# Performance work log

Hardware: AMD Instinct MI355X
Metric: run time of the kernel (lower is better)

Reference implementation:

```python
import jax, jax.numpy as jnp
import numpy as np

H = 1024
F = 132

def _lstm_cell(x, h, c, Wih, Whh, bih, bhh):
    # PyTorch LSTMCell: gates ordered i, f, g, o
    gates = x @ Wih.T + bih + h @ Whh.T + bhh  # [B, 4H]
    i, f, g, o = jnp.split(gates, 4, axis=-1)
    i = jax.nn.sigmoid(i)
    f = jax.nn.sigmoid(f)
    g = jnp.tanh(g)
    o = jax.nn.sigmoid(o)
    c_new = f * c + i * g
    h_new = o * jnp.tanh(c_new)
    return h_new, c_new


def setup_inputs() -> dict:
    key = jax.random.key(0)
    ks = jax.random.split(key, 16)
    s = 0.02
    return {
        "initial_seq": jax.random.normal(ks[0], (32, 64, F), dtype=jnp.float32),
        "generate_frames_number": 128,
        "W_ih1": jax.random.normal(ks[1], (4 * H, F), dtype=jnp.float32) * s,
        "W_hh1": jax.random.normal(ks[2], (4 * H, H), dtype=jnp.float32) * s,
        "b_ih1": jax.random.normal(ks[3], (4 * H,), dtype=jnp.float32) * s,
        "b_hh1": jax.random.normal(ks[4], (4 * H,), dtype=jnp.float32) * s,
        "W_ih2": jax.random.normal(ks[5], (4 * H, H), dtype=jnp.float32) * s,
        "W_hh2": jax.random.normal(ks[6], (4 * H, H), dtype=jnp.float32) * s,
        "b_ih2": jax.random.normal(ks[7], (4 * H,), dtype=jnp.float32) * s,
        "b_hh2": jax.random.normal(ks[8], (4 * H,), dtype=jnp.float32) * s,
        "W_ih3": jax.random.normal(ks[9], (4 * H, H), dtype=jnp.float32) * s,
        "W_hh3": jax.random.normal(ks[10], (4 * H, H), dtype=jnp.float32) * s,
        "b_ih3": jax.random.normal(ks[11], (4 * H,), dtype=jnp.float32) * s,
        "b_hh3": jax.random.normal(ks[12], (4 * H,), dtype=jnp.float32) * s,
        "W_dec": jax.random.normal(ks[13], (F, H), dtype=jnp.float32) * s,
        "b_dec": jax.random.normal(ks[14], (F,), dtype=jnp.float32) * s,
    }


def reference(initial_seq, generate_frames_number,
              W_ih1, W_hh1, b_ih1, b_hh1,
              W_ih2, W_hh2, b_ih2, b_hh2,
              W_ih3, W_hh3, b_ih3, b_hh3,
              W_dec, b_dec):
    B = initial_seq.shape[0]
    dt = initial_seq.dtype
    zeros = jnp.zeros((B, H), dtype=dt)
    state0 = (zeros, zeros, zeros, zeros, zeros, zeros)  # h0,h1,h2,c0,c1,c2

    def step(state, in_frame):
        h0, h1, h2, c0, c1, c2 = state
        h0, c0 = _lstm_cell(in_frame, h0, c0, W_ih1, W_hh1, b_ih1, b_hh1)
        h1, c1 = _lstm_cell(h0, h1, c1, W_ih2, W_hh2, b_ih2, b_hh2)
        h2, c2 = _lstm_cell(h1, h2, c2, W_ih3, W_hh3, b_ih3, b_hh3)
        out_frame = h2 @ W_dec.T + b_dec  # [B, F]
        return (h0, h1, h2, c0, c1, c2), out_frame

    # Priming pass over the conditioning sequence (outputs discarded except last)
    def prime_step(carry, in_frame):
        state, _ = carry
        state, out = step(state, in_frame)
        return (state, out), None

    init_frame = jnp.zeros((B, F), dtype=dt)
    xs = jnp.swapaxes(initial_seq, 0, 1)  # [T, B, F]
    (state, cur_frame), _ = jax.lax.scan(prime_step, (state0, init_frame), xs)

    def gen_step(carry, _):
        state, frame = carry
        state, out = step(state, frame)
        return (state, out), out

    _, outs = jax.lax.scan(gen_step, (state, cur_frame), None,
                           length=generate_frames_number)  # [N, B, F]
    return jnp.swapaxes(outs, 0, 1)  # [B, N, F]
```

## Files before the change

kernel.cpp:

```cpp
#include <hip/hip_runtime.h>
#include <stdint.h>

typedef unsigned short u16;
typedef unsigned long long u64;
typedef __attribute__((ext_vector_type(8))) short short8;
typedef __attribute__((ext_vector_type(4))) float f32x4;

#define SZ_BIGW    (4096ull*1024ull*2ull)
#define OFF_WHH1   (0ull)
#define OFF_WIH2   (OFF_WHH1 + SZ_BIGW)
#define OFF_WHH2   (OFF_WIH2 + SZ_BIGW)
#define OFF_WIH3   (OFF_WHH2 + SZ_BIGW)
#define OFF_WHH3   (OFF_WIH3 + SZ_BIGW)
#define OFF_MCOMB  (OFF_WHH3 + SZ_BIGW)
#define OFF_WIH1   (OFF_MCOMB + SZ_BIGW)
#define SZ_WIH1    (4096ull*160ull*2ull)
#define OFF_WDECF  (OFF_WIH1 + SZ_WIH1)
#define SZ_WDECF   (160ull*1024ull*2ull)
#define OFF_WDECB  (OFF_WDECF + SZ_WDECF)
#define SZ_WDECB   (1024ull*160ull*2ull)
#define OFF_XPRIM  (OFF_WDECB + SZ_WDECB)
#define SZ_XPRIM   (64ull*5120ull*2ull)
#define OFF_H2HIST (OFF_XPRIM + SZ_XPRIM)
#define SZ_HSLOT   (32768ull*2ull)
#define SZ_H2HIST  (129ull*SZ_HSLOT)
#define OFF_H0R    (OFF_H2HIST + SZ_H2HIST)
#define SZ_HR      (192ull*SZ_HSLOT)
#define OFF_H1R    (OFF_H0R + SZ_HR)
#define OFF_H2R    (OFF_H1R + SZ_HR)
#define SZ_H2R     (64ull*SZ_HSLOT)
#define OFF_ZEROH  (OFF_H2R + SZ_H2R)
#define OFF_FLAGS  (OFF_ZEROH + SZ_HSLOT)
#define SZ_FLAGS   (4096ull)
#define OFF_BS1    (OFF_FLAGS + SZ_FLAGS)
#define OFF_BS1G   (OFF_BS1 + 16384ull)
#define OFF_BS2    (OFF_BS1G + 16384ull)
#define OFF_BS3    (OFF_BS2 + 16384ull)
#define BLOB_SIZE  (OFF_BS3 + 16384ull)

__device__ unsigned char g_blob[BLOB_SIZE];

#define ZERO_BYTES (SZ_HSLOT + SZ_FLAGS)

__device__ __forceinline__ u16 f2bf(float f) {
  unsigned u = __float_as_uint(f);
  u += 0x7fffu + ((u >> 16) & 1u);
  return (u16)(u >> 16);
}
__device__ __forceinline__ float sigm(float x) { return 1.f / (1.f + __expf(-x)); }
__device__ __forceinline__ float tanh_(float x) {
  x = fminf(fmaxf(x, -40.f), 40.f);
  float e = __expf(2.f * x);
  return (e - 1.f) / (e + 1.f);
}

__global__ __launch_bounds__(256) void k_zero(uint4* p, int n) {
  int i = blockIdx.x * 256 + threadIdx.x;
  for (; i < n; i += gridDim.x * 256) p[i] = make_uint4(0u, 0u, 0u, 0u);
}

__global__ __launch_bounds__(256) void k_swizzle(const float* __restrict__ src, u16* __restrict__ dst,
                                                 int J, int Jsrc, int Kpad, int Ksrc, int srcld,
                                                 int transposed, int perm) {
  int total = J * Kpad;
  int nkc = Kpad >> 3;
  for (int o = blockIdx.x * 256 + threadIdx.x; o < total; o += gridDim.x * 256) {
    int chunk = o >> 7, within = o & 127;
    int nt = chunk / nkc, kc = chunk - nt * nkc;
    int jr = within >> 3, ke = within & 7;
    int j = perm ? ((jr >> 2) * 1024 + nt * 4 + (jr & 3)) : (nt * 16 + jr);
    int k = kc * 8 + ke;
    float v = 0.f;
    if (j < Jsrc && k < Ksrc)
      v = transposed ? src[(size_t)k * srcld + j] : src[(size_t)j * srcld + k];
    dst[o] = f2bf(v);
  }
}

__global__ __launch_bounds__(256) void k_xprim(const float* __restrict__ iseq, u16* __restrict__ dst) {
  int o = blockIdx.x * 256 + threadIdx.x;
  if (o >= 64 * 5120) return;
  int t = o / 5120, rem = o - t * 5120;
  int kc = rem >> 8, b = (rem >> 3) & 31, ke = rem & 7;
  int k = kc * 8 + ke;
  float v = (k < 132) ? iseq[(size_t)b * (64 * 132) + t * 132 + k] : 0.f;
  dst[o] = f2bf(v);
}

__global__ __launch_bounds__(256) void k_bias(const float* bih1, const float* bhh1,
                                              const float* bih2, const float* bhh2,
                                              const float* bih3, const float* bhh3,
                                              const float* __restrict__ Wih1, const float* __restrict__ bdec,
                                              float* bs1, float* bs1g, float* bs2, float* bs3) {
  int j = blockIdx.x * 256 + threadIdx.x;
  if (j >= 4096) return;
  float s1 = bih1[j] + bhh1[j];
  float bc = 0.f;
  const float* wr = Wih1 + (size_t)j * 132;
  for (int f = 0; f < 132; ++f) bc += wr[f] * bdec[f];
  bs1[j] = s1;
  bs1g[j] = s1 + bc;
  bs2[j] = bih2[j] + bhh2[j];
  bs3[j] = bih3[j] + bhh3[j];
}

__global__ __launch_bounds__(256) void k_mcomb(const u16* __restrict__ A, const u16* __restrict__ Bm,
                                               u16* __restrict__ dst) {
  int blk = blockIdx.x;
  int mt = blk & 255, jg = blk >> 8;
  int w = threadIdx.x >> 6, l = threadIdx.x & 63, q = l >> 4, r = l & 15;
  int nt = jg * 4 + w;
  f32x4 acc = {};
  for (int ks = 0; ks < 5; ++ks) {
    short8 a = *(const short8*)(A + ((size_t)mt * 20 + ks * 4 + q) * 128 + r * 8);
    short8 b = *(const short8*)(Bm + ((size_t)nt * 20 + ks * 4 + q) * 128 + r * 8);
    acc = __builtin_amdgcn_mfma_f32_16x16x32_bf16(a, b, acc, 0, 0, 0);
  }
  int kout = nt * 16 + r;
#pragma unroll
  for (int i = 0; i < 4; ++i) {
    int jrow = q * 4 + i;
    dst[(((size_t)mt * 128 + (kout >> 3)) << 7) + jrow * 8 + (kout & 7)] = f2bf(acc[i]);
  }
}


__device__ __forceinline__ void wait_all(unsigned* F, unsigned tgt) {
  if (threadIdx.x < 256) {
    while (__hip_atomic_load(F + threadIdx.x, __ATOMIC_RELAXED, __HIP_MEMORY_SCOPE_AGENT) < tgt)
      __builtin_amdgcn_s_sleep(1);
  }
  __syncthreads();
}

#define MFMA(a, b, c) __builtin_amdgcn_mfma_f32_16x16x32_bf16((a), (b), (c), 0, 0, 0)

template<int LBASE>
__device__ __forceinline__ void gen_layer(
    const u16* __restrict__ xa, const short8 (&wA)[4],
    const u16* __restrict__ xb, const short8 (&wB)[4],
    unsigned* waitF, unsigned wtgt,
    const float* __restrict__ bsum, float& creg, u16* __restrict__ hout,
    unsigned* arrF, unsigned aval,
    float (*red)[2][256], u64* hstage, int nt)
{
  int tid = threadIdx.x;
  int w = tid >> 6, l = tid & 63, q = l >> 4, r = l & 15;
  f32x4 acc0 = {}, acc1 = {};

#pragma unroll
  for (int i = 0; i < 4; ++i) {
    const u16* xp = xb + (w + 8 * i) * 1024 + q * 256 + r * 8;
    short8 a0 = *(const short8*)(xp);
    short8 a1 = *(const short8*)(xp + 128);
    acc0 = MFMA(a0, wB[i], acc0);
    acc1 = MFMA(a1, wB[i], acc1);
  }

  wait_all(waitF, wtgt);

#pragma unroll
  for (int i = 0; i < 4; ++i) {
    const u16* xp = xa + (w + 8 * i) * 1024 + q * 256 + r * 8;
    short8 a0 = *(const short8*)(xp);
    short8 a1 = *(const short8*)(xp + 128);
    acc0 = MFMA(a0, wA[i], acc0);
    acc1 = MFMA(a1, wA[i], acc1);
  }

  *(f32x4*)&red[w][0][l * 4] = acc0;
  *(f32x4*)&red[w][1][l * 4] = acc1;
  __syncthreads();

  if (tid >= LBASE && tid < LBASE + 128) {
    int idx = tid - LBASE;
    int b = idx >> 2, hl = idx & 3, mt = b >> 4, row = b & 15;
    int j0 = nt * 4 + hl;
    float g4[4];
#pragma unroll
    for (int g = 0; g < 4; ++g) {
      int col = g * 4 + hl;
      int lidx = ((row >> 2) * 16 + col) * 4 + (row & 3);
      float s = bsum[g * 1024 + j0];
#pragma unroll
      for (int ww = 0; ww < 8; ++ww) s += red[ww][mt][lidx];
      g4[g] = s;
    }
    float iv = sigm(g4[0]), fv = sigm(g4[1]), gv = tanh_(g4[2]), ov = sigm(g4[3]);
    float cn = fv * creg + iv * gv;
    creg = cn;
    ((u16*)hstage)[LBASE + idx] = f2bf(ov * tanh_(cn));
  }
  __syncthreads();

  if (tid < 64) {
    if (tid < 32) {
      u64 v = hstage[(LBASE >> 2) + tid];
      u64* dp = (u64*)(hout + ((size_t)(nt >> 1) * 256 + tid * 8 + (nt & 1) * 4));
      __hip_atomic_store(dp, v, __ATOMIC_RELAXED, __HIP_MEMORY_SCOPE_AGENT);
    }
    asm volatile("s_waitcnt vmcnt(0)" ::: "memory");
    if (tid == 0)
      __hip_atomic_store(arrF + nt, aval, __ATOMIC_RELAXED, __HIP_MEMORY_SCOPE_AGENT);
  }
}

__global__ __launch_bounds__(512, 1) void k_rnn(unsigned char* blob) {
  __shared__ float red3[3][8][2][256];
  __shared__ u64 hstage[96];
  const u16* XPRIM = (const u16*)(blob + OFF_XPRIM);
  const u16* tWIH1 = (const u16*)(blob + OFF_WIH1);
  const u16* tMCOMB = (const u16*)(blob + OFF_MCOMB);
  const u16* tWHH1 = (const u16*)(blob + OFF_WHH1);
  const u16* tWIH2 = (const u16*)(blob + OFF_WIH2);
  const u16* tWHH2 = (const u16*)(blob + OFF_WHH2);
  const u16* tWIH3 = (const u16*)(blob + OFF_WIH3);
  const u16* tWHH3 = (const u16*)(blob + OFF_WHH3);
  const float* BS1 = (const float*)(blob + OFF_BS1);
  const float* BS1G = (const float*)(blob + OFF_BS1G);
  const float* BS2 = (const float*)(blob + OFF_BS2);
  const float* BS3 = (const float*)(blob + OFF_BS3);
  u16* H0R = (u16*)(blob + OFF_H0R);
  u16* H1R = (u16*)(blob + OFF_H1R);
  u16* H2R = (u16*)(blob + OFF_H2R);
  u16* H2HIST = (u16*)(blob + OFF_H2HIST);
  const u16* ZEROH = (const u16*)(blob + OFF_ZEROH);
  unsigned* FLAGS = (unsigned*)(blob + OFF_FLAGS);
  unsigned *FP = FLAGS, *F1 = FLAGS + 256, *F2 = FLAGS + 512, *F3 = FLAGS + 768;

  int nt = blockIdx.x;
  int tid = threadIdx.x;
  int w = tid >> 6, l = tid & 63, q = l >> 4, r = l & 15;
  int layer = tid >> 7, idx = tid & 127;
  const float* BSP = (layer == 0) ? BS1 : (layer == 1) ? BS2 : BS3;
  float creg = 0.f;

  short8 rWhh1[4], rWih2[4], rWhh2[4], rWih3[4], rWhh3[4];
#pragma unroll
  for (int i = 0; i < 4; ++i) {
    size_t off = (size_t)nt * 16384 + (size_t)(w + 8 * i) * 512 + (size_t)l * 8;
    rWhh1[i] = *(const short8*)(tWHH1 + off);
    rWih2[i] = *(const short8*)(tWIH2 + off);
    rWhh2[i] = *(const short8*)(tWHH2 + off);
    rWih3[i] = *(const short8*)(tWIH3 + off);
    rWhh3[i] = *(const short8*)(tWHH3 + off);
  }
  short8 rWih1 = {};
  if (w < 5)
    rWih1 = *(const short8*)(tWIH1 + (size_t)nt * 2560 + (size_t)w * 512 + (size_t)l * 8);

  for (int b = 0; b < 66; ++b) {
    f32x4 a10 = {}, a11 = {}, a20 = {}, a21 = {}, a30 = {}, a31 = {};

    if (b < 64 && w < 5) {
      const u16* xp = XPRIM + b * 5120 + w * 1024 + q * 256 + r * 8;
      short8 x0 = *(const short8*)(xp);
      short8 x1 = *(const short8*)(xp + 128);
      a10 = MFMA(x0, rWih1, a10);
      a11 = MFMA(x1, rWih1, a11);
    }

    wait_all(FP, (unsigned)b);

    if (b <= 64) {
      const u16* h0p = (b == 0) ? ZEROH : H0R + (size_t)(b - 1) * 32768;
#pragma unroll
      for (int i = 0; i < 4; ++i) {
        const u16* xp = h0p + (w + 8 * i) * 1024 + q * 256 + r * 8;
        short8 x0 = *(const short8*)(xp);
        short8 x1 = *(const short8*)(xp + 128);
        if (b <= 63) { a10 = MFMA(x0, rWhh1[i], a10); a11 = MFMA(x1, rWhh1[i], a11); }
        if (b >= 1)  { a20 = MFMA(x0, rWih2[i], a20); a21 = MFMA(x1, rWih2[i], a21); }
      }
    }
    if (b >= 1) {
      const u16* h1p = (b == 1) ? ZEROH : H1R + (size_t)(b - 2) * 32768;
#pragma unroll
      for (int i = 0; i < 4; ++i) {
        const u16* xp = h1p + (w + 8 * i) * 1024 + q * 256 + r * 8;
        short8 x0 = *(const short8*)(xp);
        short8 x1 = *(const short8*)(xp + 128);
        if (b <= 64) { a20 = MFMA(x0, rWhh2[i], a20); a21 = MFMA(x1, rWhh2[i], a21); }
        if (b >= 2)  { a30 = MFMA(x0, rWih3[i], a30); a31 = MFMA(x1, rWih3[i], a31); }
      }
    }
    if (b >= 2) {
      const u16* h2p = (b == 2) ? ZEROH : H2R + (size_t)(b - 3) * 32768;
#pragma unroll
      for (int i = 0; i < 4; ++i) {
        const u16* xp = h2p + (w + 8 * i) * 1024 + q * 256 + r * 8;
        short8 x0 = *(const short8*)(xp);
        short8 x1 = *(const short8*)(xp + 128);
        a30 = MFMA(x0, rWhh3[i], a30);
        a31 = MFMA(x1, rWhh3[i], a31);
      }
    }

    *(f32x4*)&red3[0][w][0][l * 4] = a10;  *(f32x4*)&red3[0][w][1][l * 4] = a11;
    *(f32x4*)&red3[1][w][0][l * 4] = a20;  *(f32x4*)&red3[1][w][1][l * 4] = a21;
    *(f32x4*)&red3[2][w][0][l * 4] = a30;  *(f32x4*)&red3[2][w][1][l * 4] = a31;
    __syncthreads();

    int tb = b - layer;
    if (tid < 384 && tb >= 0 && tb <= 63) {
      int bb = idx >> 2, hl = idx & 3, mt = bb >> 4, row = bb & 15;
      int j0 = nt * 4 + hl;
      float g4[4];
#pragma unroll
      for (int g = 0; g < 4; ++g) {
        int col = g * 4 + hl;
        int lidx = ((row >> 2) * 16 + col) * 4 + (row & 3);
        float s = BSP[g * 1024 + j0];
#pragma unroll
        for (int ww = 0; ww < 8; ++ww) s += red3[layer][ww][mt][lidx];
        g4[g] = s;
      }
      float iv = sigm(g4[0]), fv = sigm(g4[1]), gv = tanh_(g4[2]), ov = sigm(g4[3]);
      float cn = fv * creg + iv * gv;
      creg = cn;
      ((u16*)hstage)[tid] = f2bf(ov * tanh_(cn));
    }
    __syncthreads();

    if (tid < 64) {
      if (tid < 32) {
        size_t doff = (size_t)(nt >> 1) * 256 + (size_t)tid * 8 + (size_t)(nt & 1) * 4;
        if (b <= 63)
          __hip_atomic_store((u64*)(H0R + (size_t)b * 32768 + doff), hstage[tid],
                             __ATOMIC_RELAXED, __HIP_MEMORY_SCOPE_AGENT);
        if (b >= 1 && b <= 64)
          __hip_atomic_store((u64*)(H1R + (size_t)(b - 1) * 32768 + doff), hstage[32 + tid],
                             __ATOMIC_RELAXED, __HIP_MEMORY_SCOPE_AGENT);
        if (b >= 2) {
          u16* dst = (b < 65) ? (H2R + (size_t)(b - 2) * 32768) : H2HIST;
          __hip_atomic_store((u64*)(dst + doff), hstage[64 + tid],
                             __ATOMIC_RELAXED, __HIP_MEMORY_SCOPE_AGENT);
        }
      }
      asm volatile("s_waitcnt vmcnt(0)" ::: "memory");
      if (tid == 0)
        __hip_atomic_store(FP + nt, (unsigned)(b + 1), __ATOMIC_RELAXED, __HIP_MEMORY_SCOPE_AGENT);
    }
  }

  short8 rMcomb[4];
#pragma unroll
  for (int i = 0; i < 4; ++i)
    rMcomb[i] = *(const short8*)(tMCOMB + (size_t)nt * 16384 + (size_t)(w + 8 * i) * 512 + (size_t)l * 8);

  for (int t = 64; t < 192; ++t) {
    gen_layer<0>(H2HIST + (size_t)(t - 64) * 32768, rMcomb,
                 H0R + (size_t)(t - 1) * 32768, rWhh1,
                 (t == 64) ? FP : F3, (t == 64) ? 66u : (unsigned)(t - 64),
                 BS1G, creg, H0R + (size_t)t * 32768,
                 F1, (unsigned)(t - 63), red3[0], hstage, nt);
    gen_layer<128>(H0R + (size_t)t * 32768, rWih2,
                   H1R + (size_t)(t - 1) * 32768, rWhh2,
                   F1, (unsigned)(t - 63),
                   BS2, creg, H1R + (size_t)t * 32768,
                   F2, (unsigned)(t - 63), red3[0], hstage, nt);
    gen_layer<256>(H1R + (size_t)t * 32768, rWih3,
                   H2HIST + (size_t)(t - 64) * 32768, rWhh3,
                   F2, (unsigned)(t - 63),
                   BS3, creg, H2HIST + (size_t)(t - 63) * 32768,
                   F3, (unsigned)(t - 63), red3[0], hstage, nt);
  }
}

__global__ __launch_bounds__(256) void k_dec(const u16* __restrict__ h2hist, const u16* __restrict__ Wd,
                                             const float* __restrict__ bdec, float* __restrict__ out) {
  int blk = blockIdx.x;
  int s = blk / 10, nt = blk - s * 10;
  const u16* x = h2hist + (size_t)(s + 1) * 32768;
  int w = threadIdx.x >> 6, l = threadIdx.x & 63, q = l >> 4, r = l & 15;
  f32x4 acc[2] = {};
  for (int ks = w; ks < 32; ks += 4) {
    const u16* xp = x + ks * 1024 + q * 256 + r * 8;
    short8 a0 = *(const short8*)(xp);
    short8 a1 = *(const short8*)(xp + 128);
    short8 bf = *(const short8*)(Wd + (((size_t)nt * 128 + ks * 4) << 7) + l * 8);
    acc[0] = __builtin_amdgcn_mfma_f32_16x16x32_bf16(a0, bf, acc[0], 0, 0, 0);
    acc[1] = __builtin_amdgcn_mfma_f32_16x16x32_bf16(a1, bf, acc[1], 0, 0, 0);
  }
  __shared__ float red[4][2][256];
#pragma unroll
  for (int mt = 0; mt < 2; ++mt)
#pragma unroll
    for (int i = 0; i < 4; ++i) red[w][mt][l * 4 + i] = acc[mt][i];
  __syncthreads();
  for (int pp = threadIdx.x; pp < 512; pp += 256) {
    int b = pp >> 4, fs = pp & 15;
    int mt = b >> 4, row = b & 15;
    int lidx = ((row >> 2) * 16 + fs) * 4 + (row & 3);
    int f = nt * 16 + fs;
    if (f < 132) {
      float v = red[0][mt][lidx] + red[1][mt][lidx] + red[2][mt][lidx] + red[3][mt][lidx] + bdec[f];
      out[(size_t)b * (128 * 132) + s * 132 + f] = v;
    }
  }
}

extern "C" void kernel_launch(void* const* d_in, const int* in_sizes, int n_in,
                              void* d_out, int out_size, void* d_ws, size_t ws_size,
                              hipStream_t stream) {
  unsigned char* blob = nullptr;
  hipGetSymbolAddress((void**)&blob, HIP_SYMBOL(g_blob));

  const float* iseq = (const float*)d_in[0];
  const float* Wih1 = (const float*)d_in[2];
  const float* Whh1 = (const float*)d_in[3];
  const float* bih1 = (const float*)d_in[4];
  const float* bhh1 = (const float*)d_in[5];
  const float* Wih2 = (const float*)d_in[6];
  const float* Whh2 = (const float*)d_in[7];
  const float* bih2 = (const float*)d_in[8];
  const float* bhh2 = (const float*)d_in[9];
  const float* Wih3 = (const float*)d_in[10];
  const float* Whh3 = (const float*)d_in[11];
  const float* bih3 = (const float*)d_in[12];
  const float* bhh3 = (const float*)d_in[13];
  const float* Wdec = (const float*)d_in[14];
  const float* bdec = (const float*)d_in[15];

  u16* tWHH1 = (u16*)(blob + OFF_WHH1);
  u16* tWIH2 = (u16*)(blob + OFF_WIH2);
  u16* tWHH2 = (u16*)(blob + OFF_WHH2);
  u16* tWIH3 = (u16*)(blob + OFF_WIH3);
  u16* tWHH3 = (u16*)(blob + OFF_WHH3);
  u16* tMCOMB = (u16*)(blob + OFF_MCOMB);
  u16* tWIH1 = (u16*)(blob + OFF_WIH1);
  u16* tWDECF = (u16*)(blob + OFF_WDECF);
  u16* tWDECB = (u16*)(blob + OFF_WDECB);
  u16* XPRIM = (u16*)(blob + OFF_XPRIM);
  u16* H2HIST = (u16*)(blob + OFF_H2HIST);
  float* BS1 = (float*)(blob + OFF_BS1);
  float* BS1G = (float*)(blob + OFF_BS1G);
  float* BS2 = (float*)(blob + OFF_BS2);
  float* BS3 = (float*)(blob + OFF_BS3);

  k_zero<<<68, 256, 0, stream>>>((uint4*)(blob + OFF_ZEROH), (int)(ZERO_BYTES / 16));
  k_swizzle<<<2048, 256, 0, stream>>>(Whh1, tWHH1, 4096, 4096, 1024, 1024, 1024, 0, 1);
  k_swizzle<<<2048, 256, 0, stream>>>(Wih2, tWIH2, 4096, 4096, 1024, 1024, 1024, 0, 1);
  k_swizzle<<<2048, 256, 0, stream>>>(Whh2, tWHH2, 4096, 4096, 1024, 1024, 1024, 0, 1);
  k_swizzle<<<2048, 256, 0, stream>>>(Wih3, tWIH3, 4096, 4096, 1024, 1024, 1024, 0, 1);
  k_swizzle<<<2048, 256, 0, stream>>>(Whh3, tWHH3, 4096, 4096, 1024, 1024, 1024, 0, 1);
  k_swizzle<<<2048, 256, 0, stream>>>(Wih1, tWIH1, 4096, 4096, 160, 132, 132, 0, 1);
  k_swizzle<<<512, 256, 0, stream>>>(Wdec, tWDECF, 160, 132, 1024, 1024, 1024, 0, 0);
  k_swizzle<<<512, 256, 0, stream>>>(Wdec, tWDECB, 1024, 1024, 160, 132, 1024, 1, 0);
  k_xprim<<<1280, 256, 0, stream>>>(iseq, XPRIM);
  k_bias<<<16, 256, 0, stream>>>(bih1, bhh1, bih2, bhh2, bih3, bhh3, Wih1, bdec, BS1, BS1G, BS2, BS3);
  k_mcomb<<<4096, 256, 0, stream>>>(tWIH1, tWDECB, tMCOMB);

  {
    void* args[] = { (void*)&blob };
    hipError_t ce = hipLaunchCooperativeKernel((void*)k_rnn, dim3(256), dim3(512), args, 0, stream);
    if (ce != hipSuccess) {
      k_rnn<<<dim3(256), dim3(512), 0, stream>>>(blob);
    }
  }

  k_dec<<<1280, 256, 0, stream>>>(H2HIST, tWDECF, bdec, (float*)d_out);
}
```

Baseline: 2.305 ms.

## Prefetch next layer's recurrent input before barrier and pipeline flag polling

```diff
diff --git a/kernel.cpp b/kernel.cpp
--- a/kernel.cpp
+++ b/kernel.cpp
@@ -125,20 +125,51 @@
 }
 
 
+__device__ __forceinline__ void poll_pipe(const unsigned* p, unsigned tgt) {
+  unsigned a, b;
+  asm volatile(
+      "global_load_dword %0, %2, off sc0 sc1\n\t"
+      "global_load_dword %1, %2, off sc0 sc1\n\t"
+      "PL0_%=:\n\t"
+      "s_waitcnt vmcnt(1)\n\t"
+      "v_cmp_lt_u32 vcc, %0, %3\n\t"
+      "s_cbranch_vccz PLD_%=\n\t"
+      "global_load_dword %0, %2, off sc0 sc1\n\t"
+      "s_waitcnt vmcnt(1)\n\t"
+      "v_cmp_lt_u32 vcc, %1, %3\n\t"
+      "s_cbranch_vccz PLD_%=\n\t"
+      "global_load_dword %1, %2, off sc0 sc1\n\t"
+      "s_branch PL0_%=\n\t"
+      "PLD_%=:\n\t"
+      "s_waitcnt vmcnt(0)\n\t"
+      : "=&v"(a), "=&v"(b)
+      : "v"(p), "v"(tgt)
+      : "vcc", "memory");
+}
+
 __device__ __forceinline__ void wait_all(unsigned* F, unsigned tgt) {
-  if (threadIdx.x < 256) {
-    while (__hip_atomic_load(F + threadIdx.x, __ATOMIC_RELAXED, __HIP_MEMORY_SCOPE_AGENT) < tgt)
-      __builtin_amdgcn_s_sleep(1);
-  }
+  if (threadIdx.x < 256) poll_pipe(F + threadIdx.x, tgt);
   __syncthreads();
 }
 
 #define MFMA(a, b, c) __builtin_amdgcn_mfma_f32_16x16x32_bf16((a), (b), (c), 0, 0, 0)
+
+struct PF { short8 v[8]; };
+
+__device__ __forceinline__ void pf_issue(PF& pf, const u16* base, int w, int q, int r) {
+#pragma unroll
+  for (int i = 0; i < 4; ++i) {
+    const u16* xp = base + (w + 8 * i) * 1024 + q * 256 + r * 8;
+    pf.v[2 * i]     = *(const short8*)(xp);
+    pf.v[2 * i + 1] = *(const short8*)(xp + 128);
+  }
+}
 
 template<int LBASE>
 __device__ __forceinline__ void gen_layer(
     const u16* __restrict__ xa, const short8 (&wA)[4],
-    const u16* __restrict__ xb, const short8 (&wB)[4],
+    const PF& pfB, const short8 (&wB)[4],
+    const u16* __restrict__ nxt, PF& pfN,
     unsigned* waitF, unsigned wtgt,
     const float* __restrict__ bsum, float& creg, u16* __restrict__ hout,
     unsigned* arrF, unsigned aval,
@@ -150,12 +181,11 @@
 
 #pragma unroll
   for (int i = 0; i < 4; ++i) {
-    const u16* xp = xb + (w + 8 * i) * 1024 + q * 256 + r * 8;
-    short8 a0 = *(const short8*)(xp);
-    short8 a1 = *(const short8*)(xp + 128);
-    acc0 = MFMA(a0, wB[i], acc0);
-    acc1 = MFMA(a1, wB[i], acc1);
-  }
+    acc0 = MFMA(pfB.v[2 * i],     wB[i], acc0);
+    acc1 = MFMA(pfB.v[2 * i + 1], wB[i], acc1);
+  }
+
+  if (nxt) pf_issue(pfN, nxt, w, q, r);
 
   wait_all(waitF, wtgt);
 
@@ -252,25 +282,29 @@
   for (int b = 0; b < 66; ++b) {
     f32x4 a10 = {}, a11 = {}, a20 = {}, a21 = {}, a30 = {}, a31 = {};
 
+    short8 x0 = {}, x1 = {};
     if (b < 64 && w < 5) {
       const u16* xp = XPRIM + b * 5120 + w * 1024 + q * 256 + r * 8;
-      short8 x0 = *(const short8*)(xp);
-      short8 x1 = *(const short8*)(xp + 128);
+      x0 = *(const short8*)(xp);
+      x1 = *(const short8*)(xp + 128);
+    }
+
+    wait_all(FP, (unsigned)b);
+
+    if (b < 64 && w < 5) {
       a10 = MFMA(x0, rWih1, a10);
       a11 = MFMA(x1, rWih1, a11);
     }
 
-    wait_all(FP, (unsigned)b);
-
     if (b <= 64) {
       const u16* h0p = (b == 0) ? ZEROH : H0R + (size_t)(b - 1) * 32768;
 #pragma unroll
       for (int i = 0; i < 4; ++i) {
         const u16* xp = h0p + (w + 8 * i) * 1024 + q * 256 + r * 8;
-        short8 x0 = *(const short8*)(xp);
-        short8 x1 = *(const short8*)(xp + 128);
-        if (b <= 63) { a10 = MFMA(x0, rWhh1[i], a10); a11 = MFMA(x1, rWhh1[i], a11); }
-        if (b >= 1)  { a20 = MFMA(x0, rWih2[i], a20); a21 = MFMA(x1, rWih2[i], a21); }
+        short8 x0_ = *(const short8*)(xp);
+        short8 x1_ = *(const short8*)(xp + 128);
+        if (b <= 63) { a10 = MFMA(x0_, rWhh1[i], a10); a11 = MFMA(x1_, rWhh1[i], a11); }
+        if (b >= 1)  { a20 = MFMA(x0_, rWih2[i], a20); a21 = MFMA(x1_, rWih2[i], a21); }
       }
     }
     if (b >= 1) {
@@ -278,10 +312,10 @@
 #pragma unroll
       for (int i = 0; i < 4; ++i) {
         const u16* xp = h1p + (w + 8 * i) * 1024 + q * 256 + r * 8;
-        short8 x0 = *(const short8*)(xp);
-        short8 x1 = *(const short8*)(xp + 128);
-        if (b <= 64) { a20 = MFMA(x0, rWhh2[i], a20); a21 = MFMA(x1, rWhh2[i], a21); }
-        if (b >= 2)  { a30 = MFMA(x0, rWih3[i], a30); a31 = MFMA(x1, rWih3[i], a31); }
+        short8 x0_ = *(const short8*)(xp);
+        short8 x1_ = *(const short8*)(xp + 128);
+        if (b <= 64) { a20 = MFMA(x0_, rWhh2[i], a20); a21 = MFMA(x1_, rWhh2[i], a21); }
+        if (b >= 2)  { a30 = MFMA(x0_, rWih3[i], a30); a31 = MFMA(x1_, rWih3[i], a31); }
       }
     }
     if (b >= 2) {
@@ -289,10 +323,10 @@
 #pragma unroll
       for (int i = 0; i < 4; ++i) {
         const u16* xp = h2p + (w + 8 * i) * 1024 + q * 256 + r * 8;
-        short8 x0 = *(const short8*)(xp);
-        short8 x1 = *(const short8*)(xp + 128);
-        a30 = MFMA(x0, rWhh3[i], a30);
-        a31 = MFMA(x1, rWhh3[i], a31);
+        short8 x0_ = *(const short8*)(xp);
+        short8 x1_ = *(const short8*)(xp + 128);
+        a30 = MFMA(x0_, rWhh3[i], a30);
+        a31 = MFMA(x1_, rWhh3[i], a31);
       }
     }
 
@@ -343,6 +377,9 @@
     }
   }
 
+  PF pf1, pf2, pf3;
+  pf_issue(pf1, H0R + (size_t)63 * 32768, w, q, r);
+
   short8 rMcomb[4];
 #pragma unroll
   for (int i = 0; i < 4; ++i)
@@ -350,17 +387,20 @@
 
   for (int t = 64; t < 192; ++t) {
     gen_layer<0>(H2HIST + (size_t)(t - 64) * 32768, rMcomb,
-                 H0R + (size_t)(t - 1) * 32768, rWhh1,
+                 pf1, rWhh1,
+                 H1R + (size_t)(t - 1) * 32768, pf2,
                  (t == 64) ? FP : F3, (t == 64) ? 66u : (unsigned)(t - 64),
                  BS1G, creg, H0R + (size_t)t * 32768,
                  F1, (unsigned)(t - 63), red3[0], hstage, nt);
     gen_layer<128>(H0R + (size_t)t * 32768, rWih2,
-                   H1R + (size_t)(t - 1) * 32768, rWhh2,
+                   pf2, rWhh2,
+                   H2HIST + (size_t)(t - 64) * 32768, pf3,
                    F1, (unsigned)(t - 63),
                    BS2, creg, H1R + (size_t)t * 32768,
                    F2, (unsigned)(t - 63), red3[0], hstage, nt);
     gen_layer<256>(H1R + (size_t)t * 32768, rWih3,
-                   H2HIST + (size_t)(t - 64) * 32768, rWhh3,
+                   pf3, rWhh3,
+                   (t < 191) ? (H0R + (size_t)t * 32768) : nullptr, pf1,
                    F2, (unsigned)(t - 63),
                    BS3, creg, H2HIST + (size_t)(t - 63) * 32768,
                    F3, (unsigned)(t - 63), red3[0], hstage, nt);
```

New measurement: 3.994 ms. 73.3% more time.
